# Kernel tuning notes

Measured on AMD Instinct MI355X. Metric: run time of the kernel, lower is better.

The kernel has to match this reference:

```python
import jax, jax.numpy as jnp
import numpy as np

B, C, H, W, HEADS = 2, 128, 56, 56, 4
ASYM_W = 0.5


def setup_inputs() -> dict:
    key = jax.random.key(0)
    ks = jax.random.split(key, 9)
    s = lambda k, shape: jax.random.normal(k, shape, jnp.float32) * 0.02
    inner = C  # dim_head * heads == dim
    return {
        "x": jax.random.normal(ks[0], (B, C, H, W), jnp.float32),
        "Wq": s(ks[1], (inner, C)),
        "Wk": s(ks[2], (inner, C)),
        "Wv": s(ks[3], (inner, C)),
        "Wo": s(ks[4], (C, inner)),
        "bo": jnp.zeros((C,), jnp.float32),
        "Wa1": s(ks[5], (C, 2 * C)),
        "ba1": jnp.zeros((C,), jnp.float32),
        "Wa2": s(ks[6], (1, C)),
        "ba2": jnp.zeros((1,), jnp.float32),
    }


def _conv1x1(Wmat, t, bias=None):
    # 1x1 conv == per-pixel matmul over channels
    out = jnp.einsum('oc,bchw->bohw', Wmat, t)
    if bias is not None:
        out = out + bias[None, :, None, None]
    return out


def reference(x, Wq, Wk, Wv, Wo, bo, Wa1, ba1, Wa2, ba2):
    b, c, h, w = x.shape
    heads = HEADS
    dh = c // heads
    scale = dh ** -0.5

    # ---- asymmetry map ----
    left = x[:, :, :, : w // 2]
    right = x[:, :, :, w // 2:]
    right_flipped = right[:, :, :, ::-1]
    mw = min(left.shape[3], right_flipped.shape[3])
    cat = jnp.concatenate([left[:, :, :, :mw], right_flipped[:, :, :, :mw]], axis=1)
    a = _conv1x1(Wa1, cat, ba1)
    a = jax.nn.gelu(a, approximate=False)  # torch default GELU is exact erf
    a = _conv1x1(Wa2, a, ba2)
    a = jax.nn.sigmoid(a)
    # bilinear, align_corners=False == half-pixel convention of jax.image.resize
    asym = jax.image.resize(a, (b, 1, h, w), method='linear')

    # ---- q/k/v projections ----
    def heads_split(t):  # b (h d) x y -> b h (x y) d
        return t.reshape(b, heads, dh, h * w).transpose(0, 1, 3, 2)

    q = heads_split(_conv1x1(Wq, x))
    k = heads_split(_conv1x1(Wk, x))
    v = heads_split(_conv1x1(Wv, x))

    dots = jnp.einsum('bhid,bhjd->bhij', q, k) * scale  # [b,h,hw,hw]

    # 3x3 neighborhood mask, vectorized
    idx = jnp.arange(h * w)
    ii, jj = idx // w, idx % w
    mask = ((jnp.abs(ii[:, None] - ii[None, :]) <= 1)
            & (jnp.abs(jj[:, None] - jj[None, :]) <= 1)).astype(dots.dtype)
    dots = dots * mask + (1.0 - mask) * -1e9

    attn = jax.nn.softmax(dots, axis=-1)
    out = jnp.einsum('bhij,bhjd->bhid', attn, v)
    out = out.transpose(0, 1, 3, 2).reshape(b, c, h, w)  # b h (x y) d -> b (h d) x y

    out = out * (1.0 + ASYM_W * asym)
    return _conv1x1(Wo, out, bo)
```

## Files before the change

kernel.cpp:

```cpp
#include <hip/hip_runtime.h>
#include <hip/hip_bf16.h>
#include <math.h>

#define B_ 2
#define C_ 128
#define H_ 56
#define W_ 56
#define N_ (H_*W_)
#define HEADS_ 4
#define DH_ 32
#define MW_ 28
#define NPOS_ (H_*MW_)

typedef __bf16 v8bf __attribute__((ext_vector_type(8)));
typedef float  v4f  __attribute__((ext_vector_type(4)));

#define MFMA16(a,b,c) __builtin_amdgcn_mfma_f32_16x16x32_bf16((a),(b),(c),0,0,0)

__device__ __forceinline__ unsigned short f2bf(float f) {
    return __builtin_bit_cast(unsigned short, __float2bfloat16(f));
}

__global__ __launch_bounds__(256)
void qkv_asym_kernel(const float* __restrict__ x,
                     const float* __restrict__ Wq, const float* __restrict__ Wk,
                     const float* __restrict__ Wv,
                     const float* __restrict__ Wa1, const float* __restrict__ ba1,
                     const float* __restrict__ Wa2, const float* __restrict__ ba2,
                     float* __restrict__ q, float* __restrict__ k,
                     float* __restrict__ v, float* __restrict__ aval) {
    __shared__ __align__(16) char smem[35840];
    const int t = threadIdx.x;
    const int b = blockIdx.z;
    const int wv_ = t >> 6;
    const int l   = t & 63;
    const int lr  = l & 15;
    const int lq  = l >> 4;

    if (blockIdx.y < 6) {
        unsigned short* WT = (unsigned short*)smem;
        unsigned short* XT = (unsigned short*)(smem + 17408);
        float* ep = (float*)smem;

        const int n0  = blockIdx.x * 64;
        const int mIdx = blockIdx.y >> 1;
        const int o0  = (blockIdx.y & 1) * 64;
        const float* W = (mIdx == 0 ? Wq : (mIdx == 1 ? Wk : Wv));
        float* dst     = (mIdx == 0 ? q  : (mIdx == 1 ? k  : v ));
        const float* xb = x + (size_t)b * C_ * N_;

        for (int it = 0; it < 8; ++it) {
            int idx = t + it * 256;
            int row = idx >> 5, f4 = idx & 31;
            float4 w4 = *(const float4*)(W + (size_t)(o0 + row) * C_ + f4 * 4);
            ushort4 p4 = { f2bf(w4.x), f2bf(w4.y), f2bf(w4.z), f2bf(w4.w) };
            *(ushort4*)(WT + row * 136 + f4 * 4) = p4;
        }
        {
            int px = t & 63, g = t >> 6;
            const float* xc = xb + n0 + px;
            for (int it = 0; it < 8; ++it) {
                int c0 = (g + it * 4) * 4;
                float a0 = xc[(size_t)(c0 + 0) * N_];
                float a1 = xc[(size_t)(c0 + 1) * N_];
                float a2 = xc[(size_t)(c0 + 2) * N_];
                float a3 = xc[(size_t)(c0 + 3) * N_];
                ushort4 p4 = { f2bf(a0), f2bf(a1), f2bf(a2), f2bf(a3) };
                *(ushort4*)(XT + px * 136 + c0) = p4;
            }
        }
        __syncthreads();

        v4f acc[4];
        #pragma unroll
        for (int nt = 0; nt < 4; ++nt) acc[nt] = (v4f){0.f, 0.f, 0.f, 0.f};

        #pragma unroll
        for (int ks = 0; ks < 4; ++ks) {
            v8bf af = *(const v8bf*)(WT + (wv_ * 16 + lr) * 136 + ks * 32 + lq * 8);
            #pragma unroll
            for (int nt = 0; nt < 4; ++nt) {
                v8bf bfr = *(const v8bf*)(XT + (nt * 16 + lr) * 136 + ks * 32 + lq * 8);
                acc[nt] = MFMA16(af, bfr, acc[nt]);
            }
        }

        __syncthreads();
        #pragma unroll
        for (int nt = 0; nt < 4; ++nt)
            #pragma unroll
            for (int r = 0; r < 4; ++r)
                ep[(nt * 16 + lr) * 68 + wv_ * 16 + lq * 4 + r] = acc[nt][r];
        __syncthreads();
        for (int it = 0; it < 4; ++it) {
            int idx = t + it * 256;
            int p = idx >> 4, f4 = idx & 15;
            *(float4*)(dst + ((size_t)b * N_ + n0 + p) * C_ + o0 + f4 * 4) =
                *(const float4*)(ep + p * 68 + f4 * 4);
        }
    } else {
        unsigned short* wa  = (unsigned short*)smem;
        unsigned short* cat = (unsigned short*)(smem + 18432);
        float* wred = (float*)(smem + 35328);

        const int P0 = blockIdx.x * 32;
        const float* xb = x + (size_t)b * C_ * N_;

        {
            int pos = t & 31, chg = t >> 5;
            int pg = P0 + pos;
            int h = pg / MW_, j = pg - h * MW_;
            int col = (chg < 4) ? (h * W_ + j) : (h * W_ + (W_ - 1 - j));
            int cbase = (chg & 3) * 32;
            const float* src = xb + col;
            unsigned short* crow = cat + pos * 264 + chg * 32;
            #pragma unroll
            for (int u = 0; u < 16; ++u) {
                float f0 = src[(size_t)(cbase + 2 * u) * N_];
                float f1 = src[(size_t)(cbase + 2 * u + 1) * N_];
                ushort2 pp = { f2bf(f0), f2bf(f1) };
                *(ushort2*)(crow + 2 * u) = pp;
            }
        }

        v4f acc2[2][2];
        #pragma unroll
        for (int mi = 0; mi < 2; ++mi)
            #pragma unroll
            for (int nt = 0; nt < 2; ++nt) acc2[mi][nt] = (v4f){0.f, 0.f, 0.f, 0.f};

        for (int kc = 0; kc < 4; ++kc) {
            __syncthreads();
            for (int it = 0; it < 8; ++it) {
                int idx = t + it * 256;
                int row = idx >> 4, f4 = idx & 15;
                float4 w4 = *(const float4*)(Wa1 + (size_t)row * 256 + kc * 64 + f4 * 4);
                ushort4 p4 = { f2bf(w4.x), f2bf(w4.y), f2bf(w4.z), f2bf(w4.w) };
                *(ushort4*)(wa + row * 72 + f4 * 4) = p4;
            }
            __syncthreads();
            #pragma unroll
            for (int ks = 0; ks < 2; ++ks) {
                v8bf a0f = *(const v8bf*)(wa + ((2*wv_ + 0) * 16 + lr) * 72 + ks * 32 + lq * 8);
                v8bf a1f = *(const v8bf*)(wa + ((2*wv_ + 1) * 16 + lr) * 72 + ks * 32 + lq * 8);
                v8bf b0f = *(const v8bf*)(cat + lr * 264        + kc * 64 + ks * 32 + lq * 8);
                v8bf b1f = *(const v8bf*)(cat + (16 + lr) * 264 + kc * 64 + ks * 32 + lq * 8);
                acc2[0][0] = MFMA16(a0f, b0f, acc2[0][0]);
                acc2[0][1] = MFMA16(a0f, b1f, acc2[0][1]);
                acc2[1][0] = MFMA16(a1f, b0f, acc2[1][0]);
                acc2[1][1] = MFMA16(a1f, b1f, acc2[1][1]);
            }
        }

        float p2[2] = {0.f, 0.f};
        #pragma unroll
        for (int mi = 0; mi < 2; ++mi) {
            #pragma unroll
            for (int r = 0; r < 4; ++r) {
                int m = (2*wv_ + mi) * 16 + lq * 4 + r;
                float wa2v = Wa2[m];
                float b1v  = ba1[m];
                #pragma unroll
                for (int nt = 0; nt < 2; ++nt) {
                    float val = acc2[mi][nt][r] + b1v;
                    float gl = 0.5f * val * (1.0f + erff(val * 0.7071067811865475f));
                    p2[nt] += gl * wa2v;
                }
            }
        }
        #pragma unroll
        for (int nt = 0; nt < 2; ++nt) {
            p2[nt] += __shfl_xor(p2[nt], 16, 64);
            p2[nt] += __shfl_xor(p2[nt], 32, 64);
        }
        if (l < 16) {
            wred[wv_ * 32 + lr]      = p2[0];
            wred[wv_ * 32 + 16 + lr] = p2[1];
        }
        __syncthreads();
        if (t < 32) {
            float s = wred[t] + wred[32 + t] + wred[64 + t] + wred[96 + t] + ba2[0];
            aval[(size_t)b * NPOS_ + P0 + t] = 1.0f / (1.0f + expf(-s));
        }
    }
}

__global__ __launch_bounds__(256)
void attn_kernel(const float* __restrict__ q, const float* __restrict__ k,
                 const float* __restrict__ v, const float* __restrict__ aval,
                 float* __restrict__ ao) {
    const int gid = blockIdx.x * 256 + threadIdx.x;
    const int s    = gid & 3;
    const int rest = gid >> 2;
    const int n    = rest % N_;
    const int hb   = rest / N_;
    const int head = hb & (HEADS_ - 1);
    const int b    = hb >> 2;
    const int i = n / W_, j = n - i * W_;
    const int dbase = head * DH_ + s * 8;

    const float* qp = q + ((size_t)b * N_ + n) * C_ + dbase;
    const float4 q0 = *(const float4*)qp;
    const float4 q1 = *(const float4*)(qp + 4);

    float dts[9];
    int   mm[9];
    #pragma unroll
    for (int tt = 0; tt < 9; ++tt) {
        int di = tt / 3 - 1, dj = tt % 3 - 1;
        int ii = i + di, jj = j + dj;
        bool ok = ((unsigned)ii < (unsigned)H_) && ((unsigned)jj < (unsigned)W_);
        int m = ok ? ii * W_ + jj : n;
        mm[tt] = m;
        const float* kp = k + ((size_t)b * N_ + m) * C_ + dbase;
        float4 k0 = *(const float4*)kp;
        float4 k1 = *(const float4*)(kp + 4);
        float pd = q0.x*k0.x + q0.y*k0.y + q0.z*k0.z + q0.w*k0.w
                 + q1.x*k1.x + q1.y*k1.y + q1.z*k1.z + q1.w*k1.w;
        pd += __shfl_xor(pd, 1, 64);
        pd += __shfl_xor(pd, 2, 64);
        dts[tt] = ok ? pd * 0.17677669529663687f : -1e30f;
    }
    float mx = dts[0];
    #pragma unroll
    for (int tt = 1; tt < 9; ++tt) mx = fmaxf(mx, dts[tt]);
    float sum = 0.f;
    #pragma unroll
    for (int tt = 0; tt < 9; ++tt) { dts[tt] = expf(dts[tt] - mx); sum += dts[tt]; }
    const float inv = 1.0f / sum;

    float4 a0 = {0,0,0,0}, a1 = {0,0,0,0};
    #pragma unroll
    for (int tt = 0; tt < 9; ++tt) {
        const float* vp = v + ((size_t)b * N_ + mm[tt]) * C_ + dbase;
        float4 v0 = *(const float4*)vp;
        float4 v1 = *(const float4*)(vp + 4);
        float wt = dts[tt] * inv;
        a0.x += wt * v0.x; a0.y += wt * v0.y; a0.z += wt * v0.z; a0.w += wt * v0.w;
        a1.x += wt * v1.x; a1.y += wt * v1.y; a1.z += wt * v1.z; a1.w += wt * v1.w;
    }

    float f = 0.5f * (float)j - 0.25f;
    f = fminf(fmaxf(f, 0.0f), 27.0f);
    int i0 = (int)f; if (i0 > 26) i0 = 26;
    float frac = f - (float)i0;
    const float* av = aval + (size_t)b * NPOS_ + i * MW_;
    float a = av[i0] * (1.0f - frac) + av[i0 + 1] * frac;
    float sc = 1.0f + 0.5f * a;

    float* op = ao + ((size_t)b * N_ + n) * C_ + dbase;
    float4 r0 = { a0.x*sc, a0.y*sc, a0.z*sc, a0.w*sc };
    float4 r1 = { a1.x*sc, a1.y*sc, a1.z*sc, a1.w*sc };
    *(float4*)op       = r0;
    *(float4*)(op + 4) = r1;
}

__global__ __launch_bounds__(256)
void oproj_kernel(const float* __restrict__ ao, const float* __restrict__ Wo,
                  const float* __restrict__ bo, float* __restrict__ out) {
    __shared__ __align__(16) char smem[34816];
    unsigned short* WT = (unsigned short*)smem;
    unsigned short* XT = (unsigned short*)(smem + 17408);
    float* ep = (float*)smem;

    const int t = threadIdx.x;
    const int n0 = blockIdx.x * 64;
    const int o0 = blockIdx.y * 64;
    const int b  = blockIdx.z;
    const int wv_ = t >> 6, l = t & 63, lr = l & 15, lq = l >> 4;

    for (int it = 0; it < 8; ++it) {
        int idx = t + it * 256;
        int row = idx >> 5, f4 = idx & 31;
        float4 w4 = *(const float4*)(Wo + (size_t)(o0 + row) * C_ + f4 * 4);
        ushort4 p4 = { f2bf(w4.x), f2bf(w4.y), f2bf(w4.z), f2bf(w4.w) };
        *(ushort4*)(WT + row * 136 + f4 * 4) = p4;
    }
    for (int it = 0; it < 8; ++it) {
        int idx = t + it * 256;
        int row = idx >> 5, f4 = idx & 31;
        float4 a4 = *(const float4*)(ao + ((size_t)b * N_ + n0 + row) * C_ + f4 * 4);
        ushort4 p4 = { f2bf(a4.x), f2bf(a4.y), f2bf(a4.z), f2bf(a4.w) };
        *(ushort4*)(XT + row * 136 + f4 * 4) = p4;
    }
    __syncthreads();

    v4f acc[4];
    #pragma unroll
    for (int nt = 0; nt < 4; ++nt) acc[nt] = (v4f){0.f, 0.f, 0.f, 0.f};

    #pragma unroll
    for (int ks = 0; ks < 4; ++ks) {
        v8bf af = *(const v8bf*)(WT + (wv_ * 16 + lr) * 136 + ks * 32 + lq * 8);
        #pragma unroll
        for (int nt = 0; nt < 4; ++nt) {
            v8bf bfr = *(const v8bf*)(XT + (nt * 16 + lr) * 136 + ks * 32 + lq * 8);
            acc[nt] = MFMA16(af, bfr, acc[nt]);
        }
    }

    __syncthreads();
    const float4 bv = *(const float4*)(bo + o0 + wv_ * 16 + lq * 4);
    const float bvr[4] = { bv.x, bv.y, bv.z, bv.w };
    #pragma unroll
    for (int nt = 0; nt < 4; ++nt)
        #pragma unroll
        for (int r = 0; r < 4; ++r)
            ep[(wv_ * 16 + lq * 4 + r) * 68 + nt * 16 + lr] = acc[nt][r] + bvr[r];
    __syncthreads();
    for (int it = 0; it < 4; ++it) {
        int idx = t + it * 256;
        int o = idx >> 4, f4 = idx & 15;
        *(float4*)(out + (size_t)b * C_ * N_ + (size_t)(o0 + o) * N_ + n0 + f4 * 4) =
            *(const float4*)(ep + o * 68 + f4 * 4);
    }
}

extern "C" void kernel_launch(void* const* d_in, const int* in_sizes, int n_in,
                              void* d_out, int out_size, void* d_ws, size_t ws_size,
                              hipStream_t stream) {
    const float* x   = (const float*)d_in[0];
    const float* Wq  = (const float*)d_in[1];
    const float* Wk  = (const float*)d_in[2];
    const float* Wv  = (const float*)d_in[3];
    const float* Wo  = (const float*)d_in[4];
    const float* bo  = (const float*)d_in[5];
    const float* Wa1 = (const float*)d_in[6];
    const float* ba1 = (const float*)d_in[7];
    const float* Wa2 = (const float*)d_in[8];
    const float* ba2 = (const float*)d_in[9];
    float* out = (float*)d_out;

    const size_t PXC = (size_t)B_ * N_ * C_;
    float* q    = (float*)d_ws;
    float* k    = q + PXC;
    float* v    = k + PXC;
    float* ao   = v + PXC;
    float* aval = ao + PXC;

    qkv_asym_kernel<<<dim3(49, 7, B_), 256, 0, stream>>>(
        x, Wq, Wk, Wv, Wa1, ba1, Wa2, ba2, q, k, v, aval);
    attn_kernel<<<(B_ * HEADS_ * N_ * 4) / 256, 256, 0, stream>>>(q, k, v, aval, ao);
    oproj_kernel<<<dim3(49, 2, B_), 256, 0, stream>>>(ao, Wo, bo, out);
}
```

Before: 96.92 us.

## Fuse attention with output projection, store QKV in bf16, pre-transpose x

Adds a pre-pass that transposes x into a pixel-major bf16 buffer, so the QKV and asymmetry stages read contiguous vectors instead of strided per-channel scalars. Q/K/V are now written as bf16, which halves intermediate traffic. The attention kernel is fused with the output projection, so the attention output stays in shared memory rather than going through a global fp32 buffer and a separate kernel. The cost is an extra launch for the transpose, more precision loss in Q/K/V, and each block reloading the full Wo with a smaller 32-pixel tile.

After: 102.6 us. 5.9% more time.

```diff
diff --git a/kernel.cpp b/kernel.cpp
--- a/kernel.cpp
+++ b/kernel.cpp
@@ -12,6 +12,7 @@
 #define MW_ 28
 #define NPOS_ (H_*MW_)
 
+typedef unsigned short ushort_t;
 typedef __bf16 v8bf __attribute__((ext_vector_type(8)));
 typedef float  v4f  __attribute__((ext_vector_type(4)));
 
@@ -20,15 +21,56 @@
 __device__ __forceinline__ unsigned short f2bf(float f) {
     return __builtin_bit_cast(unsigned short, __float2bfloat16(f));
 }
+__device__ __forceinline__ unsigned int bfpack(float a, float b) {
+    return (unsigned int)f2bf(a) | ((unsigned int)f2bf(b) << 16);
+}
+__device__ __forceinline__ void unpack8(uint4 u, float* f) {
+    f[0] = __uint_as_float(u.x << 16); f[1] = __uint_as_float(u.x & 0xffff0000u);
+    f[2] = __uint_as_float(u.y << 16); f[3] = __uint_as_float(u.y & 0xffff0000u);
+    f[4] = __uint_as_float(u.z << 16); f[5] = __uint_as_float(u.z & 0xffff0000u);
+    f[6] = __uint_as_float(u.w << 16); f[7] = __uint_as_float(u.w & 0xffff0000u);
+}
 
 __global__ __launch_bounds__(256)
-void qkv_asym_kernel(const float* __restrict__ x,
+void xpose_kernel(const float* __restrict__ x, ushort_t* __restrict__ xbf) {
+    __shared__ float xs[128 * 68];
+    const int t  = threadIdx.x;
+    const int n0 = blockIdx.x * 64;
+    const int b  = blockIdx.y;
+    const float* xb = x + (size_t)b * C_ * N_;
+
+    for (int it = 0; it < 8; ++it) {
+        int idx = t + it * 256;
+        int c = idx >> 4, f4 = idx & 15;
+        *(float4*)(&xs[c * 68 + f4 * 4]) =
+            *(const float4*)(xb + (size_t)c * N_ + n0 + f4 * 4);
+    }
+    __syncthreads();
+    const int rot = t & 7;
+    for (int it = 0; it < 4; ++it) {
+        int task = t + it * 256;
+        int ug = task & 15, px = task >> 4;
+        float f[8];
+        #pragma unroll
+        for (int s = 0; s < 8; ++s) {
+            int u = (s + rot) & 7;
+            f[u] = xs[(ug * 8 + u) * 68 + px];
+        }
+        uint4 o;
+        o.x = bfpack(f[0], f[1]); o.y = bfpack(f[2], f[3]);
+        o.z = bfpack(f[4], f[5]); o.w = bfpack(f[6], f[7]);
+        *(uint4*)(xbf + ((size_t)b * N_ + n0 + px) * C_ + ug * 8) = o;
+    }
+}
+
+__global__ __launch_bounds__(256)
+void qkv_asym_kernel(const ushort_t* __restrict__ xbf,
                      const float* __restrict__ Wq, const float* __restrict__ Wk,
                      const float* __restrict__ Wv,
                      const float* __restrict__ Wa1, const float* __restrict__ ba1,
                      const float* __restrict__ Wa2, const float* __restrict__ ba2,
-                     float* __restrict__ q, float* __restrict__ k,
-                     float* __restrict__ v, float* __restrict__ aval) {
+                     ushort_t* __restrict__ q, ushort_t* __restrict__ k,
+                     ushort_t* __restrict__ v, float* __restrict__ aval) {
     __shared__ __align__(16) char smem[35840];
     const int t = threadIdx.x;
     const int b = blockIdx.z;
@@ -38,16 +80,14 @@
     const int lq  = l >> 4;
 
     if (blockIdx.y < 6) {
-        unsigned short* WT = (unsigned short*)smem;
-        unsigned short* XT = (unsigned short*)(smem + 17408);
-        float* ep = (float*)smem;
-
-        const int n0  = blockIdx.x * 64;
+        ushort_t* WT = (ushort_t*)smem;
+        ushort_t* XT = (ushort_t*)(smem + 17408);
+
+        const int n0   = blockIdx.x * 64;
         const int mIdx = blockIdx.y >> 1;
-        const int o0  = (blockIdx.y & 1) * 64;
-        const float* W = (mIdx == 0 ? Wq : (mIdx == 1 ? Wk : Wv));
-        float* dst     = (mIdx == 0 ? q  : (mIdx == 1 ? k  : v ));
-        const float* xb = x + (size_t)b * C_ * N_;
+        const int o0   = (blockIdx.y & 1) * 64;
+        const float* W  = (mIdx == 0 ? Wq : (mIdx == 1 ? Wk : Wv));
+        ushort_t* dst   = (mIdx == 0 ? q  : (mIdx == 1 ? k  : v ));
 
         for (int it = 0; it < 8; ++it) {
             int idx = t + it * 256;
@@ -56,18 +96,11 @@
             ushort4 p4 = { f2bf(w4.x), f2bf(w4.y), f2bf(w4.z), f2bf(w4.w) };
             *(ushort4*)(WT + row * 136 + f4 * 4) = p4;
         }
-        {
-            int px = t & 63, g = t >> 6;
-            const float* xc = xb + n0 + px;
-            for (int it = 0; it < 8; ++it) {
-                int c0 = (g + it * 4) * 4;
-                float a0 = xc[(size_t)(c0 + 0) * N_];
-                float a1 = xc[(size_t)(c0 + 1) * N_];
-                float a2 = xc[(size_t)(c0 + 2) * N_];
-                float a3 = xc[(size_t)(c0 + 3) * N_];
-                ushort4 p4 = { f2bf(a0), f2bf(a1), f2bf(a2), f2bf(a3) };
-                *(ushort4*)(XT + px * 136 + c0) = p4;
-            }
+        for (int it = 0; it < 4; ++it) {
+            int idx = t + it * 256;
+            int px = idx >> 4, g = idx & 15;
+            uint4 r = *(const uint4*)(xbf + ((size_t)b * N_ + n0 + px) * C_ + g * 8);
+            *(uint4*)(XT + px * 136 + g * 8) = r;
         }
         __syncthreads();
 
@@ -86,41 +119,36 @@
         }
 
         __syncthreads();
-        #pragma unroll
-        for (int nt = 0; nt < 4; ++nt)
-            #pragma unroll
-            for (int r = 0; r < 4; ++r)
-                ep[(nt * 16 + lr) * 68 + wv_ * 16 + lq * 4 + r] = acc[nt][r];
+        ushort_t* epT = WT;
+        #pragma unroll
+        for (int nt = 0; nt < 4; ++nt) {
+            uint2 pk;
+            pk.x = bfpack(acc[nt][0], acc[nt][1]);
+            pk.y = bfpack(acc[nt][2], acc[nt][3]);
+            *(uint2*)(epT + (nt * 16 + lr) * 136 + wv_ * 16 + lq * 4) = pk;
+        }
         __syncthreads();
+        for (int it = 0; it < 2; ++it) {
+            int idx = t + it * 256;
+            int px = idx >> 3, g = idx & 7;
+            *(uint4*)(dst + ((size_t)b * N_ + n0 + px) * C_ + o0 + g * 8) =
+                *(const uint4*)(epT + px * 136 + g * 8);
+        }
+    } else {
+        ushort_t* wa  = (ushort_t*)smem;
+        ushort_t* cat = (ushort_t*)(smem + 18432);
+        float* wred   = (float*)(smem + 35328);
+
+        const int P0 = blockIdx.x * 32;
+
         for (int it = 0; it < 4; ++it) {
             int idx = t + it * 256;
-            int p = idx >> 4, f4 = idx & 15;
-            *(float4*)(dst + ((size_t)b * N_ + n0 + p) * C_ + o0 + f4 * 4) =
-                *(const float4*)(ep + p * 68 + f4 * 4);
-        }
-    } else {
-        unsigned short* wa  = (unsigned short*)smem;
-        unsigned short* cat = (unsigned short*)(smem + 18432);
-        float* wred = (float*)(smem + 35328);
-
-        const int P0 = blockIdx.x * 32;
-        const float* xb = x + (size_t)b * C_ * N_;
-
-        {
-            int pos = t & 31, chg = t >> 5;
+            int pos = idx >> 5, g = idx & 31;
             int pg = P0 + pos;
             int h = pg / MW_, j = pg - h * MW_;
-            int col = (chg < 4) ? (h * W_ + j) : (h * W_ + (W_ - 1 - j));
-            int cbase = (chg & 3) * 32;
-            const float* src = xb + col;
-            unsigned short* crow = cat + pos * 264 + chg * 32;
-            #pragma unroll
-            for (int u = 0; u < 16; ++u) {
-                float f0 = src[(size_t)(cbase + 2 * u) * N_];
-                float f1 = src[(size_t)(cbase + 2 * u + 1) * N_];
-                ushort2 pp = { f2bf(f0), f2bf(f1) };
-                *(ushort2*)(crow + 2 * u) = pp;
-            }
+            int n = h * W_ + ((g < 16) ? j : (W_ - 1 - j));
+            uint4 r = *(const uint4*)(xbf + ((size_t)b * N_ + n) * C_ + (g & 15) * 8);
+            *(uint4*)(cat + pos * 264 + g * 8) = r;
         }
 
         v4f acc2[2][2];
@@ -186,133 +214,126 @@
 }
 
 __global__ __launch_bounds__(256)
-void attn_kernel(const float* __restrict__ q, const float* __restrict__ k,
-                 const float* __restrict__ v, const float* __restrict__ aval,
-                 float* __restrict__ ao) {
-    const int gid = blockIdx.x * 256 + threadIdx.x;
-    const int s    = gid & 3;
-    const int rest = gid >> 2;
-    const int n    = rest % N_;
-    const int hb   = rest / N_;
-    const int head = hb & (HEADS_ - 1);
-    const int b    = hb >> 2;
-    const int i = n / W_, j = n - i * W_;
-    const int dbase = head * DH_ + s * 8;
-
-    const float* qp = q + ((size_t)b * N_ + n) * C_ + dbase;
-    const float4 q0 = *(const float4*)qp;
-    const float4 q1 = *(const float4*)(qp + 4);
-
-    float dts[9];
-    int   mm[9];
-    #pragma unroll
-    for (int tt = 0; tt < 9; ++tt) {
-        int di = tt / 3 - 1, dj = tt % 3 - 1;
-        int ii = i + di, jj = j + dj;
-        bool ok = ((unsigned)ii < (unsigned)H_) && ((unsigned)jj < (unsigned)W_);
-        int m = ok ? ii * W_ + jj : n;
-        mm[tt] = m;
-        const float* kp = k + ((size_t)b * N_ + m) * C_ + dbase;
-        float4 k0 = *(const float4*)kp;
-        float4 k1 = *(const float4*)(kp + 4);
-        float pd = q0.x*k0.x + q0.y*k0.y + q0.z*k0.z + q0.w*k0.w
-                 + q1.x*k1.x + q1.y*k1.y + q1.z*k1.z + q1.w*k1.w;
-        pd += __shfl_xor(pd, 1, 64);
-        pd += __shfl_xor(pd, 2, 64);
-        dts[tt] = ok ? pd * 0.17677669529663687f : -1e30f;
-    }
-    float mx = dts[0];
-    #pragma unroll
-    for (int tt = 1; tt < 9; ++tt) mx = fmaxf(mx, dts[tt]);
-    float sum = 0.f;
-    #pragma unroll
-    for (int tt = 0; tt < 9; ++tt) { dts[tt] = expf(dts[tt] - mx); sum += dts[tt]; }
-    const float inv = 1.0f / sum;
-
-    float4 a0 = {0,0,0,0}, a1 = {0,0,0,0};
-    #pragma unroll
-    for (int tt = 0; tt < 9; ++tt) {
-        const float* vp = v + ((size_t)b * N_ + mm[tt]) * C_ + dbase;
-        float4 v0 = *(const float4*)vp;
-        float4 v1 = *(const float4*)(vp + 4);
-        float wt = dts[tt] * inv;
-        a0.x += wt * v0.x; a0.y += wt * v0.y; a0.z += wt * v0.z; a0.w += wt * v0.w;
-        a1.x += wt * v1.x; a1.y += wt * v1.y; a1.z += wt * v1.z; a1.w += wt * v1.w;
-    }
-
-    float f = 0.5f * (float)j - 0.25f;
-    f = fminf(fmaxf(f, 0.0f), 27.0f);
-    int i0 = (int)f; if (i0 > 26) i0 = 26;
-    float frac = f - (float)i0;
-    const float* av = aval + (size_t)b * NPOS_ + i * MW_;
-    float a = av[i0] * (1.0f - frac) + av[i0 + 1] * frac;
-    float sc = 1.0f + 0.5f * a;
-
-    float* op = ao + ((size_t)b * N_ + n) * C_ + dbase;
-    float4 r0 = { a0.x*sc, a0.y*sc, a0.z*sc, a0.w*sc };
-    float4 r1 = { a1.x*sc, a1.y*sc, a1.z*sc, a1.w*sc };
-    *(float4*)op       = r0;
-    *(float4*)(op + 4) = r1;
-}
-
-__global__ __launch_bounds__(256)
-void oproj_kernel(const float* __restrict__ ao, const float* __restrict__ Wo,
-                  const float* __restrict__ bo, float* __restrict__ out) {
-    __shared__ __align__(16) char smem[34816];
-    unsigned short* WT = (unsigned short*)smem;
-    unsigned short* XT = (unsigned short*)(smem + 17408);
-    float* ep = (float*)smem;
-
-    const int t = threadIdx.x;
-    const int n0 = blockIdx.x * 64;
-    const int o0 = blockIdx.y * 64;
-    const int b  = blockIdx.z;
-    const int wv_ = t >> 6, l = t & 63, lr = l & 15, lq = l >> 4;
-
-    for (int it = 0; it < 8; ++it) {
+void attn_oproj_kernel(const ushort_t* __restrict__ q, const ushort_t* __restrict__ k,
+                       const ushort_t* __restrict__ v, const float* __restrict__ aval,
+                       const float* __restrict__ Wo, const float* __restrict__ bo,
+                       float* __restrict__ out) {
+    __shared__ __align__(16) char smem[53248];
+    ushort_t* WoT = (ushort_t*)smem;
+    ushort_t* aoT = (ushort_t*)(smem + 34816);
+    float*    ep  = (float*)(smem + 34816);
+
+    const int t  = threadIdx.x;
+    const int n0 = blockIdx.x * 32;
+    const int b  = blockIdx.y;
+
+    for (int it = 0; it < 16; ++it) {
         int idx = t + it * 256;
         int row = idx >> 5, f4 = idx & 31;
-        float4 w4 = *(const float4*)(Wo + (size_t)(o0 + row) * C_ + f4 * 4);
+        float4 w4 = *(const float4*)(Wo + (size_t)row * C_ + f4 * 4);
         ushort4 p4 = { f2bf(w4.x), f2bf(w4.y), f2bf(w4.z), f2bf(w4.w) };
-        *(ushort4*)(WT + row * 136 + f4 * 4) = p4;
-    }
-    for (int it = 0; it < 8; ++it) {
-        int idx = t + it * 256;
-        int row = idx >> 5, f4 = idx & 31;
-        float4 a4 = *(const float4*)(ao + ((size_t)b * N_ + n0 + row) * C_ + f4 * 4);
-        ushort4 p4 = { f2bf(a4.x), f2bf(a4.y), f2bf(a4.z), f2bf(a4.w) };
-        *(ushort4*)(XT + row * 136 + f4 * 4) = p4;
+        *(ushort4*)(WoT + row * 136 + f4 * 4) = p4;
+    }
+
+    const size_t base = (size_t)b * N_ * C_;
+    for (int u = 0; u < 2; ++u) {
+        int task = t + u * 256;
+        int s = task & 3, head = (task >> 2) & 3, p = task >> 4;
+        int n = n0 + p;
+        int i = n / W_, j = n - i * W_;
+        int dbase = head * DH_ + s * 8;
+
+        float qf[8];
+        unpack8(*(const uint4*)(q + base + (size_t)n * C_ + dbase), qf);
+
+        float dts[9]; int mm[9];
+        #pragma unroll
+        for (int tt = 0; tt < 9; ++tt) {
+            int di = tt / 3 - 1, dj = tt % 3 - 1;
+            int ii = i + di, jj = j + dj;
+            bool ok = ((unsigned)ii < (unsigned)H_) && ((unsigned)jj < (unsigned)W_);
+            int m = ok ? ii * W_ + jj : n;
+            mm[tt] = m;
+            float kf[8];
+            unpack8(*(const uint4*)(k + base + (size_t)m * C_ + dbase), kf);
+            float pd = qf[0]*kf[0] + qf[1]*kf[1] + qf[2]*kf[2] + qf[3]*kf[3]
+                     + qf[4]*kf[4] + qf[5]*kf[5] + qf[6]*kf[6] + qf[7]*kf[7];
+            pd += __shfl_xor(pd, 1, 64);
+            pd += __shfl_xor(pd, 2, 64);
+            dts[tt] = ok ? pd * 0.17677669529663687f : -1e30f;
+        }
+        float mx = dts[0];
+        #pragma unroll
+        for (int tt = 1; tt < 9; ++tt) mx = fmaxf(mx, dts[tt]);
+        float sum = 0.f;
+        #pragma unroll
+        for (int tt = 0; tt < 9; ++tt) { dts[tt] = expf(dts[tt] - mx); sum += dts[tt]; }
+        const float inv = 1.0f / sum;
+
+        float acc[8] = {0,0,0,0,0,0,0,0};
+        #pragma unroll
+        for (int tt = 0; tt < 9; ++tt) {
+            float vf[8];
+            unpack8(*(const uint4*)(v + base + (size_t)mm[tt] * C_ + dbase), vf);
+            float wt = dts[tt] * inv;
+            #pragma unroll
+            for (int d = 0; d < 8; ++d) acc[d] += wt * vf[d];
+        }
+
+        float f = 0.5f * (float)j - 0.25f;
+        f = fminf(fmaxf(f, 0.0f), 27.0f);
+        int i0 = (int)f; if (i0 > 26) i0 = 26;
+        float frac = f - (float)i0;
+        const float* av = aval + (size_t)b * NPOS_ + i * MW_;
+        float a = av[i0] * (1.0f - frac) + av[i0 + 1] * frac;
+        float sc = 1.0f + 0.5f * a;
+
+        uint4 o;
+        o.x = bfpack(acc[0] * sc, acc[1] * sc);
+        o.y = bfpack(acc[2] * sc, acc[3] * sc);
+        o.z = bfpack(acc[4] * sc, acc[5] * sc);
+        o.w = bfpack(acc[6] * sc, acc[7] * sc);
+        *(uint4*)(aoT + p * 136 + dbase) = o;
     }
     __syncthreads();
 
-    v4f acc[4];
+    const int wv_ = t >> 6, l = t & 63, lr = l & 15, lq = l >> 4;
+    v4f acc4[2][2];
     #pragma unroll
-    for (int nt = 0; nt < 4; ++nt) acc[nt] = (v4f){0.f, 0.f, 0.f, 0.f};
+    for (int mi = 0; mi < 2; ++mi)
+        #pragma unroll
+        for (int nt = 0; nt < 2; ++nt) acc4[mi][nt] = (v4f){0.f, 0.f, 0.f, 0.f};
 
     #pragma unroll
     for (int ks = 0; ks < 4; ++ks) {
-        v8bf af = *(const v8bf*)(WT + (wv_ * 16 + lr) * 136 + ks * 32 + lq * 8);
-        #pragma unroll
-        for (int nt = 0; nt < 4; ++nt) {
-            v8bf bfr = *(const v8bf*)(XT + (nt * 16 + lr) * 136 + ks * 32 + lq * 8);
-            acc[nt] = MFMA16(af, bfr, acc[nt]);
-        }
-    }
-
+        v8bf b0 = *(const v8bf*)(aoT + lr * 136        + ks * 32 + lq * 8);
+        v8bf b1 = *(const v8bf*)(aoT + (16 + lr) * 136 + ks * 32 + lq * 8);
+        #pragma unroll
+        for (int mi = 0; mi < 2; ++mi) {
+            v8bf af = *(const v8bf*)(WoT + ((wv_ * 2 + mi) * 16 + lr) * 136 + ks * 32 + lq * 8);
+            acc4[mi][0] = MFMA16(af, b0, acc4[mi][0]);
+            acc4[mi][1] = MFMA16(af, b1, acc4[mi][1]);
+        }
+    }
     __syncthreads();
-    const float4 bv = *(const float4*)(bo + o0 + wv_ * 16 + lq * 4);
-    const float bvr[4] = { bv.x, bv.y, bv.z, bv.w };
+
     #pragma unroll
-    for (int nt = 0; nt < 4; ++nt)
-        #pragma unroll
-        for (int r = 0; r < 4; ++r)
-            ep[(wv_ * 16 + lq * 4 + r) * 68 + nt * 16 + lr] = acc[nt][r] + bvr[r];
+    for (int mi = 0; mi < 2; ++mi) {
+        int o = (wv_ * 2 + mi) * 16 + lq * 4;
+        float4 bv = *(const float4*)(bo + o);
+        const float bvr[4] = { bv.x, bv.y, bv.z, bv.w };
+        #pragma unroll
+        for (int nt = 0; nt < 2; ++nt)
+            #pragma unroll
+            for (int r = 0; r < 4; ++r)
+                ep[(o + r) * 36 + nt * 16 + lr] = acc4[mi][nt][r] + bvr[r];
+    }
     __syncthreads();
     for (int it = 0; it < 4; ++it) {
         int idx = t + it * 256;
-        int o = idx >> 4, f4 = idx & 15;
-        *(float4*)(out + (size_t)b * C_ * N_ + (size_t)(o0 + o) * N_ + n0 + f4 * 4) =
-            *(const float4*)(ep + o * 68 + f4 * 4);
+        int o = idx >> 3, f4 = idx & 7;
+        *(float4*)(out + (size_t)b * C_ * N_ + (size_t)o * N_ + n0 + f4 * 4) =
+            *(const float4*)(ep + o * 36 + f4 * 4);
     }
 }
 
@@ -332,14 +353,14 @@
     float* out = (float*)d_out;
 
     const size_t PXC = (size_t)B_ * N_ * C_;
-    float* q    = (float*)d_ws;
-    float* k    = q + PXC;
-    float* v    = k + PXC;
-    float* ao   = v + PXC;
-    float* aval = ao + PXC;
-
+    ushort_t* qb  = (ushort_t*)d_ws;
+    ushort_t* kb  = qb + PXC;
+    ushort_t* vb  = kb + PXC;
+    ushort_t* xbf = vb + PXC;
+    float*    aval = (float*)(xbf + PXC);
+
+    xpose_kernel   <<<dim3(49, B_), 256, 0, stream>>>(x, xbf);
     qkv_asym_kernel<<<dim3(49, 7, B_), 256, 0, stream>>>(
-        x, Wq, Wk, Wv, Wa1, ba1, Wa2, ba2, q, k, v, aval);
-    attn_kernel<<<(B_ * HEADS_ * N_ * 4) / 256, 256, 0, stream>>>(q, k, v, aval, ao);
-    oproj_kernel<<<dim3(49, 2, B_), 256, 0, stream>>>(ao, Wo, bo, out);
-}
+        xbf, Wq, Wk, Wv, Wa1, ba1, Wa2, ba2, qb, kb, vb, aval);
+    attn_oproj_kernel<<<dim3(98, B_), 256, 0, stream>>>(qb, kb, vb, aval, Wo, bo, out);
+}
```
